# Kernel tuning notes

Measured on AMD Instinct MI355X. Metric: run time of the kernel, lower is better.

The kernel has to match this reference:

```python
import jax, jax.numpy as jnp
import numpy as np

B, L, D = 1, 4096, 1024
N_AR, N_DIFF, D_HEAD = 8, 8, 64
H = N_AR + N_DIFF
ROPE_BASE = 10000.0


def rotate_half(x):
    x1, x2 = jnp.split(x, 2, axis=-1)
    return jnp.concatenate([-x2, x1], axis=-1)


def rope_cos_sin(seq_len, d_head):
    inv_freq = 1.0 / (ROPE_BASE ** (jnp.arange(0, d_head, 2, dtype=jnp.float32) / d_head))
    t = jnp.arange(seq_len, dtype=jnp.float32)
    freqs = t[:, None] * inv_freq[None, :]          # [L, d_head//2]
    emb = jnp.concatenate([freqs, freqs], axis=-1)  # [L, d_head]
    return jnp.cos(emb), jnp.sin(emb)


def setup_inputs() -> dict:
    key = jax.random.key(0)
    ks = jax.random.split(key, 5)
    return {
        "hidden_states": jax.random.normal(ks[0], (B, L, D), dtype=jnp.float32),
        "Wq": jax.random.normal(ks[1], (D, H * D_HEAD), dtype=jnp.float32) * 0.02,
        "Wk": jax.random.normal(ks[2], (D, H * D_HEAD), dtype=jnp.float32) * 0.02,
        "Wv": jax.random.normal(ks[3], (D, H * D_HEAD), dtype=jnp.float32) * 0.02,
        "Wo": jax.random.normal(ks[4], (H * D_HEAD, D), dtype=jnp.float32) * 0.02,
    }


def _attend(q, k, v, mask):
    # q,k,v: [B, h, L, d]; mask: [L, L] additive
    scale = D_HEAD ** -0.5
    scores = jnp.einsum("bhqd,bhkd->bhqk", q, k) * scale + mask
    attn = jax.nn.softmax(scores.astype(jnp.float32), axis=-1).astype(q.dtype)
    return jnp.einsum("bhqk,bhkd->bhqd", attn, v)


def reference(hidden_states, Wq, Wk, Wv, Wo):
    b, l, _ = hidden_states.shape

    def heads(x, W):
        return (x @ W).reshape(b, l, H, D_HEAD).transpose(0, 2, 1, 3)  # [B,H,L,d]

    q = heads(hidden_states, Wq)
    k = heads(hidden_states, Wk)
    v = heads(hidden_states, Wv)

    cos, sin = rope_cos_sin(l, D_HEAD)  # [L, d]
    q = q * cos + rotate_half(q) * sin
    k = k * cos + rotate_half(k) * sin

    neg_inf = jnp.finfo(jnp.float32).min
    causal = jnp.where(jnp.tril(jnp.ones((l, l), dtype=bool)), 0.0, -jnp.inf).astype(jnp.float32)

    out_ar = _attend(q[:, :N_AR], k[:, :N_AR], v[:, :N_AR], causal)
    out_diff = _attend(q[:, N_AR:], k[:, N_AR:], v[:, N_AR:], jnp.zeros((l, l), jnp.float32))

    out = jnp.concatenate([out_ar, out_diff], axis=1)          # [B,H,L,d]
    out = out.transpose(0, 2, 1, 3).reshape(b, l, H * D_HEAD)  # [B,L,H*d]
    return out @ Wo
```

## Files before the change

kernel.cpp:

```cpp
#include <hip/hip_runtime.h>

#define LSEQ 4096
#define DMODEL 1024
#define HTOT 16
#define NAR 8
#define DHEAD 64
#define QKVS 3072

typedef unsigned short u16;
typedef unsigned int u32;
typedef __attribute__((ext_vector_type(8))) short bf16x8;
typedef __attribute__((ext_vector_type(4))) float f32x4;

typedef __attribute__((address_space(1))) void gvoid;
typedef __attribute__((address_space(3))) void lvoid;

__device__ __forceinline__ void cp16(const void* g, void* l) {
    __builtin_amdgcn_global_load_lds((gvoid*)(void*)g, (lvoid*)l, 16, 0, 0);
}

__device__ __forceinline__ float bfs(u16 v) { return __uint_as_float((u32)v << 16); }
__device__ __forceinline__ u16 f2bf(float f) {
    u32 x = __float_as_uint(f);
    return (u16)((x + 0x7fffu + ((x >> 16) & 1u)) >> 16);
}
__device__ __forceinline__ u32 pack2(float a, float b) {
    return (u32)f2bf(a) | ((u32)f2bf(b) << 16);
}

__global__ __launch_bounds__(256) void transp_cvt3(
    const float* __restrict__ Wq, const float* __restrict__ Wk,
    const float* __restrict__ Wv, u16* __restrict__ D)
{
    __shared__ u16 T[64][72];
    const float* S = (blockIdx.z == 0) ? Wq : ((blockIdx.z == 1) ? Wk : Wv);
    u16* Dz = D + (size_t)blockIdx.z * 1024 * 1024;
    const int tid = threadIdx.x;
    const int bx = blockIdx.x, by = blockIdx.y;
#pragma unroll
    for (int i = 0; i < 4; ++i) {
        int id = tid + i * 256;
        int fr = id >> 4, fc = id & 15;
        float4 v = *(const float4*)(S + (size_t)(by * 64 + fr) * 1024 + bx * 64 + fc * 4);
        T[fc * 4 + 0][fr] = f2bf(v.x);
        T[fc * 4 + 1][fr] = f2bf(v.y);
        T[fc * 4 + 2][fr] = f2bf(v.z);
        T[fc * 4 + 3][fr] = f2bf(v.w);
    }
    __syncthreads();
#pragma unroll
    for (int i = 0; i < 2; ++i) {
        int id = tid + i * 256;
        int c = id >> 3, g = id & 7;
        *(uint4*)(Dz + (size_t)(bx * 64 + c) * 1024 + by * 64 + g * 8) = *(const uint4*)&T[c][g * 8];
    }
}

__global__ __launch_bounds__(256) void transp_cvt(
    const float* __restrict__ S, u16* __restrict__ D)
{
    __shared__ u16 T[64][72];
    const int tid = threadIdx.x;
    const int bx = blockIdx.x, by = blockIdx.y;
#pragma unroll
    for (int i = 0; i < 4; ++i) {
        int id = tid + i * 256;
        int fr = id >> 4, fc = id & 15;
        float4 v = *(const float4*)(S + (size_t)(by * 64 + fr) * 1024 + bx * 64 + fc * 4);
        T[fc * 4 + 0][fr] = f2bf(v.x);
        T[fc * 4 + 1][fr] = f2bf(v.y);
        T[fc * 4 + 2][fr] = f2bf(v.z);
        T[fc * 4 + 3][fr] = f2bf(v.w);
    }
    __syncthreads();
#pragma unroll
    for (int i = 0; i < 2; ++i) {
        int id = tid + i * 256;
        int c = id >> 3, g = id & 7;
        *(uint4*)(D + (size_t)(bx * 64 + c) * 1024 + by * 64 + g * 8) = *(const uint4*)&T[c][g * 8];
    }
}

__global__ __launch_bounds__(256) void gemm_qkv(
    const float* __restrict__ A, const u16* __restrict__ Bt, u16* __restrict__ C)
{
    __shared__ u16 As[2][128][40];
    __shared__ u16 Bs[2][128][32];
    const int tid = threadIdx.x;
    const int lane = tid & 63, w = tid >> 6;
    const int col = lane & 15, quad = lane >> 4;
    const int bm = blockIdx.y << 7, bn = blockIdx.x << 7;
    const int wm = (w & 1) << 6, wn = (w >> 1) << 6;
    const int sr = lane >> 2, sc = (lane & 3) << 3;
    const int ar0 = tid >> 2, ag = (tid & 3) << 3;
    const f32x4 zero = {0.f, 0.f, 0.f, 0.f};
    f32x4 acc[4][4];
#pragma unroll
    for (int i = 0; i < 4; ++i)
#pragma unroll
        for (int j = 0; j < 4; ++j) acc[i][j] = zero;

    {
#pragma unroll
        for (int i = 0; i < 2; ++i)
            cp16(Bt + (size_t)(bn + w * 32 + i * 16 + sr) * 1024 + sc, &Bs[0][w * 32 + i * 16][0]);
        float4 a0[2], a1[2];
#pragma unroll
        for (int it = 0; it < 2; ++it) {
            const float* ap = A + (size_t)(bm + ar0 + it * 64) * 1024 + ag;
            a0[it] = *(const float4*)ap;
            a1[it] = *(const float4*)(ap + 4);
        }
#pragma unroll
        for (int it = 0; it < 2; ++it) {
            uint4 pk;
            pk.x = pack2(a0[it].x, a0[it].y); pk.y = pack2(a0[it].z, a0[it].w);
            pk.z = pack2(a1[it].x, a1[it].y); pk.w = pack2(a1[it].z, a1[it].w);
            *(uint4*)&As[0][ar0 + it * 64][ag] = pk;
        }
    }

    for (int kc = 0; kc < 32; ++kc) {
        const int cur = kc & 1, nxt = cur ^ 1;
        __syncthreads();
        const bool pre = (kc + 1 < 32);
        float4 a0[2], a1[2];
        if (pre) {
            const int k1 = (kc + 1) * 32;
#pragma unroll
            for (int i = 0; i < 2; ++i)
                cp16(Bt + (size_t)(bn + w * 32 + i * 16 + sr) * 1024 + k1 + sc,
                     &Bs[nxt][w * 32 + i * 16][0]);
#pragma unroll
            for (int it = 0; it < 2; ++it) {
                const float* ap = A + (size_t)(bm + ar0 + it * 64) * 1024 + k1 + ag;
                a0[it] = *(const float4*)ap;
                a1[it] = *(const float4*)(ap + 4);
            }
        }
        bf16x8 af[4], bfr[4];
#pragma unroll
        for (int i = 0; i < 4; ++i) af[i] = *(const bf16x8*)&As[cur][wm + i * 16 + col][quad * 8];
#pragma unroll
        for (int j = 0; j < 4; ++j) bfr[j] = *(const bf16x8*)&Bs[cur][wn + j * 16 + col][quad * 8];
#pragma unroll
        for (int i = 0; i < 4; ++i)
#pragma unroll
            for (int j = 0; j < 4; ++j)
                acc[i][j] = __builtin_amdgcn_mfma_f32_16x16x32_bf16(af[i], bfr[j], acc[i][j], 0, 0, 0);
        if (pre) {
#pragma unroll
            for (int it = 0; it < 2; ++it) {
                uint4 pk;
                pk.x = pack2(a0[it].x, a0[it].y); pk.y = pack2(a0[it].z, a0[it].w);
                pk.z = pack2(a1[it].x, a1[it].y); pk.w = pack2(a1[it].z, a1[it].w);
                *(uint4*)&As[nxt][ar0 + it * 64][ag] = pk;
            }
        }
    }
#pragma unroll
    for (int i = 0; i < 4; ++i)
#pragma unroll
        for (int j = 0; j < 4; ++j)
#pragma unroll
            for (int r = 0; r < 4; ++r)
                C[(size_t)(bm + wm + i * 16 + quad * 4 + r) * QKVS + bn + wn + j * 16 + col] =
                    f2bf(acc[i][j][r]);
}

__global__ __launch_bounds__(256) void gemm_out(
    const u16* __restrict__ A, const u16* __restrict__ Bt, float* __restrict__ C)
{
    __shared__ u16 As[2][128][32];
    __shared__ u16 Bs[2][128][32];
    const int tid = threadIdx.x;
    const int lane = tid & 63, w = tid >> 6;
    const int col = lane & 15, quad = lane >> 4;
    const int bm = blockIdx.y << 7, bn = blockIdx.x << 7;
    const int wm = (w & 1) << 6, wn = (w >> 1) << 6;
    const int sr = lane >> 2, sc = (lane & 3) << 3;
    const f32x4 zero = {0.f, 0.f, 0.f, 0.f};
    f32x4 acc[4][4];
#pragma unroll
    for (int i = 0; i < 4; ++i)
#pragma unroll
        for (int j = 0; j < 4; ++j) acc[i][j] = zero;

#pragma unroll
    for (int i = 0; i < 2; ++i) {
        const int r0 = w * 32 + i * 16;
        cp16(A  + (size_t)(bm + r0 + sr) * 1024 + sc, &As[0][r0][0]);
        cp16(Bt + (size_t)(bn + r0 + sr) * 1024 + sc, &Bs[0][r0][0]);
    }

    for (int kc = 0; kc < 32; ++kc) {
        const int cur = kc & 1, nxt = cur ^ 1;
        __syncthreads();
        if (kc + 1 < 32) {
            const int k1 = (kc + 1) * 32;
#pragma unroll
            for (int i = 0; i < 2; ++i) {
                const int r0 = w * 32 + i * 16;
                cp16(A  + (size_t)(bm + r0 + sr) * 1024 + k1 + sc, &As[nxt][r0][0]);
                cp16(Bt + (size_t)(bn + r0 + sr) * 1024 + k1 + sc, &Bs[nxt][r0][0]);
            }
        }
        bf16x8 af[4], bfr[4];
#pragma unroll
        for (int i = 0; i < 4; ++i) af[i] = *(const bf16x8*)&As[cur][wm + i * 16 + col][quad * 8];
#pragma unroll
        for (int j = 0; j < 4; ++j) bfr[j] = *(const bf16x8*)&Bs[cur][wn + j * 16 + col][quad * 8];
#pragma unroll
        for (int i = 0; i < 4; ++i)
#pragma unroll
            for (int j = 0; j < 4; ++j)
                acc[i][j] = __builtin_amdgcn_mfma_f32_16x16x32_bf16(af[i], bfr[j], acc[i][j], 0, 0, 0);
    }
#pragma unroll
    for (int i = 0; i < 4; ++i)
#pragma unroll
        for (int j = 0; j < 4; ++j)
#pragma unroll
            for (int r = 0; r < 4; ++r)
                C[(size_t)(bm + wm + i * 16 + quad * 4 + r) * 1024 + bn + wn + j * 16 + col] =
                    acc[i][j][r];
}

__global__ __launch_bounds__(256) void rope_kernel(u16* __restrict__ QKV)
{
    const int idx = blockIdx.x * 256 + threadIdx.x;
    const int i = idx & 31;
    const int h = (idx >> 5) & 15;
    const int t = idx >> 9;
    const float inv = __expf((float)i * -0.2878231366242557f);
    float s, c;
    __sincosf((float)t * inv, &s, &c);
    const size_t base = (size_t)t * QKVS + h * DHEAD + i;
    const float qs = 0.18033688011112042f;

    float q1 = bfs(QKV[base]), q2 = bfs(QKV[base + 32]);
    QKV[base]      = f2bf((q1 * c - q2 * s) * qs);
    QKV[base + 32] = f2bf((q2 * c + q1 * s) * qs);

    const size_t kb = base + 1024;
    float k1 = bfs(QKV[kb]), k2 = bfs(QKV[kb + 32]);
    QKV[kb]      = f2bf(k1 * c - k2 * s);
    QKV[kb + 32] = f2bf(k2 * c + k1 * s);
}

__global__ __launch_bounds__(256) void attn_mfma(
    const u16* __restrict__ QKV, u16* __restrict__ AO)
{
    __shared__ u16 Ks[2][64][64];
    __shared__ u16 Vt[2][80][72];
    __shared__ u16 Ps[4][32][72];
    const int bid = blockIdx.x;
    int h, qt;
    if (bid < 256) { h = 8 + (bid & 7); qt = bid >> 3; }
    else { int i = bid - 256; h = i & 7; qt = 31 - (i >> 3); }
    const bool causal = (h < NAR);
    const int tid = threadIdx.x;
    const int w = tid >> 6, lane = tid & 63;
    const int col = lane & 15, quad = lane >> 4;
    const int qbase = qt * 128 + w * 32;

    {
        int row = 64 + (tid >> 4);
        u32 val = (row == 64) ? 0x3F803F80u : 0u;
        u32* p0 = (u32*)&Vt[0][row][(tid & 15) * 4];
        u32* p1 = (u32*)&Vt[1][row][(tid & 15) * 4];
        p0[0] = val; p0[1] = val; p1[0] = val; p1[1] = val;
    }

    bf16x8 qf[2][2];
#pragma unroll
    for (int im = 0; im < 2; ++im)
#pragma unroll
        for (int ks = 0; ks < 2; ++ks)
            qf[im][ks] = *(const bf16x8*)(QKV + (size_t)(qbase + im * 16 + col) * QKVS +
                                          h * DHEAD + ks * 32 + quad * 8);

    const f32x4 zero = {0.f, 0.f, 0.f, 0.f};
    f32x4 O[2][5];
#pragma unroll
    for (int im = 0; im < 2; ++im)
#pragma unroll
        for (int nd = 0; nd < 5; ++nd) O[im][nd] = zero;

    const int nch = causal ? (qt * 2 + 2) : (LSEQ / 64);
    const int kv_kp = tid & 31, kv_dg = tid >> 5;
    u16* pb = &Ps[w][quad * 4][col];
    const int krow = lane >> 3;
    const int kcb = (lane & 7) ^ krow;
    const u16* kbase = QKV + (size_t)krow * QKVS + 1024 + h * DHEAD + kcb * 8;

    {
#pragma unroll
        for (int i = 0; i < 2; ++i)
            cp16(kbase + (size_t)((i * 4 + w) * 8) * QKVS, &Ks[0][(i * 4 + w) * 8][0]);
        const u16* vp = QKV + (size_t)(kv_kp * 2) * QKVS + 2048 + h * DHEAD + kv_dg * 8;
        bf16x8 v0 = *(const bf16x8*)vp;
        bf16x8 v1 = *(const bf16x8*)(vp + QKVS);
#pragma unroll
        for (int j = 0; j < 8; ++j)
            *(u32*)&Vt[0][kv_dg * 8 + j][kv_kp * 2] = (u32)(u16)v0[j] | ((u32)(u16)v1[j] << 16);
    }

    for (int ch = 0; ch < nch; ++ch) {
        const int cur = ch & 1, nxt = cur ^ 1;
        __syncthreads();
        const bool pre = (ch + 1 < nch);
        bf16x8 v0 = {}, v1 = {};
        if (pre) {
            const int c1 = (ch + 1) * 64;
#pragma unroll
            for (int i = 0; i < 2; ++i)
                cp16(kbase + (size_t)(c1 + (i * 4 + w) * 8) * QKVS, &Ks[nxt][(i * 4 + w) * 8][0]);
            const u16* vp = QKV + (size_t)(c1 + kv_kp * 2) * QKVS + 2048 + h * DHEAD + kv_dg * 8;
            v0 = *(const bf16x8*)vp;
            v1 = *(const bf16x8*)(vp + QKVS);
        }

        f32x4 s[2][4];
#pragma unroll
        for (int im = 0; im < 2; ++im)
#pragma unroll
            for (int jn = 0; jn < 4; ++jn) s[im][jn] = zero;
#pragma unroll
        for (int jn = 0; jn < 4; ++jn)
#pragma unroll
            for (int ks = 0; ks < 2; ++ks) {
                bf16x8 kf = *(const bf16x8*)&Ks[cur][jn * 16 + col][((ks * 4 + quad) ^ (col & 7)) * 8];
                s[0][jn] = __builtin_amdgcn_mfma_f32_16x16x32_bf16(qf[0][ks], kf, s[0][jn], 0, 0, 0);
                s[1][jn] = __builtin_amdgcn_mfma_f32_16x16x32_bf16(qf[1][ks], kf, s[1][jn], 0, 0, 0);
            }
        if (causal && ch * 64 + 63 > qbase) {
#pragma unroll
            for (int im = 0; im < 2; ++im)
#pragma unroll
                for (int jn = 0; jn < 4; ++jn) {
                    int kk = ch * 64 + jn * 16 + col;
#pragma unroll
                    for (int r = 0; r < 4; ++r) {
                        int qq = qbase + im * 16 + quad * 4 + r;
                        if (kk > qq) s[im][jn][r] = -1e30f;
                    }
                }
        }
#pragma unroll
        for (int im = 0; im < 2; ++im)
#pragma unroll
            for (int jn = 0; jn < 4; ++jn)
#pragma unroll
                for (int r = 0; r < 4; ++r)
                    pb[(im * 16 + r) * 72 + jn * 16] =
                        f2bf(__builtin_amdgcn_exp2f(s[im][jn][r]));
#pragma unroll
        for (int ks = 0; ks < 2; ++ks) {
            bf16x8 pa0 = *(const bf16x8*)&Ps[w][col][ks * 32 + quad * 8];
            bf16x8 pa1 = *(const bf16x8*)&Ps[w][16 + col][ks * 32 + quad * 8];
#pragma unroll
            for (int nd = 0; nd < 5; ++nd) {
                bf16x8 vf = *(const bf16x8*)&Vt[cur][nd * 16 + col][ks * 32 + quad * 8];
                O[0][nd] = __builtin_amdgcn_mfma_f32_16x16x32_bf16(pa0, vf, O[0][nd], 0, 0, 0);
                O[1][nd] = __builtin_amdgcn_mfma_f32_16x16x32_bf16(pa1, vf, O[1][nd], 0, 0, 0);
            }
        }
        if (pre) {
#pragma unroll
            for (int j = 0; j < 8; ++j)
                *(u32*)&Vt[nxt][kv_dg * 8 + j][kv_kp * 2] =
                    (u32)(u16)v0[j] | ((u32)(u16)v1[j] << 16);
        }
    }
#pragma unroll
    for (int im = 0; im < 2; ++im)
#pragma unroll
        for (int r = 0; r < 4; ++r) {
            float l = __shfl(O[im][4][r], 0, 16);
            float inv = 1.f / l;
            int row = im * 16 + quad * 4 + r;
#pragma unroll
            for (int nd = 0; nd < 4; ++nd)
                Ps[w][row][nd * 16 + col] = f2bf(O[im][nd][r] * inv);
        }
#pragma unroll
    for (int i = 0; i < 4; ++i) {
        int id = lane + i * 64;
        int row = id >> 3, g = id & 7;
        *(uint4*)(AO + (size_t)(qt * 128 + w * 32 + row) * 1024 + h * DHEAD + g * 8) =
            *(const uint4*)&Ps[w][row][g * 8];
    }
}

extern "C" void kernel_launch(void* const* d_in, const int* in_sizes, int n_in,
                              void* d_out, int out_size, void* d_ws, size_t ws_size,
                              hipStream_t stream)
{
    const float* X  = (const float*)d_in[0];
    const float* Wq = (const float*)d_in[1];
    const float* Wk = (const float*)d_in[2];
    const float* Wv = (const float*)d_in[3];
    const float* Wo = (const float*)d_in[4];
    float* out = (float*)d_out;

    u16* Wt  = (u16*)d_ws;
    u16* AOb = (u16*)d_ws;
    u16* QKV = (u16*)d_ws + (size_t)4 * 1024 * 1024;
    u16* Wot = QKV;

    transp_cvt3<<<dim3(16, 16, 3), 256, 0, stream>>>(Wq, Wk, Wv, Wt);
    gemm_qkv<<<dim3(24, 32), 256, 0, stream>>>(X, Wt, QKV);
    rope_kernel<<<(LSEQ * HTOT * 32) / 256, 256, 0, stream>>>(QKV);
    attn_mfma<<<512, 256, 0, stream>>>(QKV, AOb);
    transp_cvt<<<dim3(16, 16), 256, 0, stream>>>(Wo, Wot);
    gemm_out<<<dim3(8, 32), 256, 0, stream>>>(AOb, Wot, out);
}
```

Measured before the change: 292.9 us.

## Compute transposed scores to keep P in registers, halve query tile per block

The attention kernel now computes S^T = K·Q^T, so each lane holds the probabilities in the B-operand layout of the 16x16x16 MFMA. P·V then runs straight from registers, with no shared-memory staging of P and no LDS round trip for the output. Each block now covers 64 queries (16 per wave) instead of 128, doubling the grid to 1024 blocks. Causal tiles are ordered in alternating short/long pairs to balance load. The row sum is computed by an MFMA against a ones vector. In exchange, each K/V tile loaded into shared memory is reused by fewer queries, so global-to-LDS traffic per query roughly doubles.

```diff
diff --git a/kernel.cpp b/kernel.cpp
--- a/kernel.cpp
+++ b/kernel.cpp
@@ -10,6 +10,7 @@
 typedef unsigned short u16;
 typedef unsigned int u32;
 typedef __attribute__((ext_vector_type(8))) short bf16x8;
+typedef __attribute__((ext_vector_type(4))) short bf16x4;
 typedef __attribute__((ext_vector_type(4))) float f32x4;
 
 typedef __attribute__((address_space(1))) void gvoid;
@@ -252,44 +253,37 @@
     const u16* __restrict__ QKV, u16* __restrict__ AO)
 {
     __shared__ u16 Ks[2][64][64];
-    __shared__ u16 Vt[2][80][72];
-    __shared__ u16 Ps[4][32][72];
+    __shared__ u16 Vt[2][64][72];
     const int bid = blockIdx.x;
     int h, qt;
-    if (bid < 256) { h = 8 + (bid & 7); qt = bid >> 3; }
-    else { int i = bid - 256; h = i & 7; qt = 31 - (i >> 3); }
+    if (bid < 512) { h = 8 + (bid & 7); qt = bid >> 3; }
+    else {
+        int i = bid - 512; h = i & 7; int j = i >> 3;
+        qt = (j & 1) ? (63 - (j >> 1)) : (j >> 1);
+    }
     const bool causal = (h < NAR);
     const int tid = threadIdx.x;
     const int w = tid >> 6, lane = tid & 63;
     const int col = lane & 15, quad = lane >> 4;
-    const int qbase = qt * 128 + w * 32;
-
-    {
-        int row = 64 + (tid >> 4);
-        u32 val = (row == 64) ? 0x3F803F80u : 0u;
-        u32* p0 = (u32*)&Vt[0][row][(tid & 15) * 4];
-        u32* p1 = (u32*)&Vt[1][row][(tid & 15) * 4];
-        p0[0] = val; p0[1] = val; p1[0] = val; p1[1] = val;
-    }
-
-    bf16x8 qf[2][2];
-#pragma unroll
-    for (int im = 0; im < 2; ++im)
-#pragma unroll
-        for (int ks = 0; ks < 2; ++ks)
-            qf[im][ks] = *(const bf16x8*)(QKV + (size_t)(qbase + im * 16 + col) * QKVS +
-                                          h * DHEAD + ks * 32 + quad * 8);
+    const int qb = qt * 64;
+    const int qrow = qb + w * 16 + col;
+
+    bf16x8 qf[2];
+#pragma unroll
+    for (int ks = 0; ks < 2; ++ks)
+        qf[ks] = *(const bf16x8*)(QKV + (size_t)qrow * QKVS + h * DHEAD + ks * 32 + quad * 8);
+
+    bf16x4 ones;
+    ones[0] = (short)0x3F80; ones[1] = (short)0x3F80;
+    ones[2] = (short)0x3F80; ones[3] = (short)0x3F80;
 
     const f32x4 zero = {0.f, 0.f, 0.f, 0.f};
-    f32x4 O[2][5];
-#pragma unroll
-    for (int im = 0; im < 2; ++im)
-#pragma unroll
-        for (int nd = 0; nd < 5; ++nd) O[im][nd] = zero;
-
-    const int nch = causal ? (qt * 2 + 2) : (LSEQ / 64);
+    f32x4 O[5];
+#pragma unroll
+    for (int nd = 0; nd < 5; ++nd) O[nd] = zero;
+
+    const int nch = causal ? (qt + 1) : (LSEQ / 64);
     const int kv_kp = tid & 31, kv_dg = tid >> 5;
-    u16* pb = &Ps[w][quad * 4][col];
     const int krow = lane >> 3;
     const int kcb = (lane & 7) ^ krow;
     const u16* kbase = QKV + (size_t)krow * QKVS + 1024 + h * DHEAD + kcb * 8;
@@ -321,51 +315,44 @@
             v1 = *(const bf16x8*)(vp + QKVS);
         }
 
-        f32x4 s[2][4];
-#pragma unroll
-        for (int im = 0; im < 2; ++im)
-#pragma unroll
-            for (int jn = 0; jn < 4; ++jn) s[im][jn] = zero;
+        f32x4 st[4];
+#pragma unroll
+        for (int jn = 0; jn < 4; ++jn) st[jn] = zero;
 #pragma unroll
         for (int jn = 0; jn < 4; ++jn)
 #pragma unroll
             for (int ks = 0; ks < 2; ++ks) {
                 bf16x8 kf = *(const bf16x8*)&Ks[cur][jn * 16 + col][((ks * 4 + quad) ^ (col & 7)) * 8];
-                s[0][jn] = __builtin_amdgcn_mfma_f32_16x16x32_bf16(qf[0][ks], kf, s[0][jn], 0, 0, 0);
-                s[1][jn] = __builtin_amdgcn_mfma_f32_16x16x32_bf16(qf[1][ks], kf, s[1][jn], 0, 0, 0);
-            }
-        if (causal && ch * 64 + 63 > qbase) {
-#pragma unroll
-            for (int im = 0; im < 2; ++im)
-#pragma unroll
-                for (int jn = 0; jn < 4; ++jn) {
-                    int kk = ch * 64 + jn * 16 + col;
-#pragma unroll
-                    for (int r = 0; r < 4; ++r) {
-                        int qq = qbase + im * 16 + quad * 4 + r;
-                        if (kk > qq) s[im][jn][r] = -1e30f;
-                    }
-                }
-        }
-#pragma unroll
-        for (int im = 0; im < 2; ++im)
-#pragma unroll
-            for (int jn = 0; jn < 4; ++jn)
+                st[jn] = __builtin_amdgcn_mfma_f32_16x16x32_bf16(kf, qf[ks], st[jn], 0, 0, 0);
+            }
+        if (causal && ch * 64 + 63 > qb + w * 16) {
+#pragma unroll
+            for (int jn = 0; jn < 4; ++jn) {
+                int kk = ch * 64 + jn * 16 + quad * 4;
 #pragma unroll
                 for (int r = 0; r < 4; ++r)
-                    pb[(im * 16 + r) * 72 + jn * 16] =
-                        f2bf(__builtin_amdgcn_exp2f(s[im][jn][r]));
-#pragma unroll
-        for (int ks = 0; ks < 2; ++ks) {
-            bf16x8 pa0 = *(const bf16x8*)&Ps[w][col][ks * 32 + quad * 8];
-            bf16x8 pa1 = *(const bf16x8*)&Ps[w][16 + col][ks * 32 + quad * 8];
-#pragma unroll
-            for (int nd = 0; nd < 5; ++nd) {
-                bf16x8 vf = *(const bf16x8*)&Vt[cur][nd * 16 + col][ks * 32 + quad * 8];
-                O[0][nd] = __builtin_amdgcn_mfma_f32_16x16x32_bf16(pa0, vf, O[0][nd], 0, 0, 0);
-                O[1][nd] = __builtin_amdgcn_mfma_f32_16x16x32_bf16(pa1, vf, O[1][nd], 0, 0, 0);
-            }
-        }
+                    if (kk + r > qrow) st[jn][r] = -1e30f;
+            }
+        }
+        bf16x4 pf[4];
+#pragma unroll
+        for (int jn = 0; jn < 4; ++jn) {
+            pf[jn][0] = (short)f2bf(__builtin_amdgcn_exp2f(st[jn][0]));
+            pf[jn][1] = (short)f2bf(__builtin_amdgcn_exp2f(st[jn][1]));
+            pf[jn][2] = (short)f2bf(__builtin_amdgcn_exp2f(st[jn][2]));
+            pf[jn][3] = (short)f2bf(__builtin_amdgcn_exp2f(st[jn][3]));
+        }
+#pragma unroll
+        for (int nd = 0; nd < 4; ++nd)
+#pragma unroll
+            for (int jn = 0; jn < 4; ++jn) {
+                bf16x4 vtf = *(const bf16x4*)&Vt[cur][nd * 16 + col][jn * 16 + quad * 4];
+                O[nd] = __builtin_amdgcn_mfma_f32_16x16x16bf16_1k(vtf, pf[jn], O[nd], 0, 0, 0);
+            }
+#pragma unroll
+        for (int jn = 0; jn < 4; ++jn)
+            O[4] = __builtin_amdgcn_mfma_f32_16x16x16bf16_1k(ones, pf[jn], O[4], 0, 0, 0);
+
         if (pre) {
 #pragma unroll
             for (int j = 0; j < 8; ++j)
@@ -373,23 +360,15 @@
                     (u32)(u16)v0[j] | ((u32)(u16)v1[j] << 16);
         }
     }
-#pragma unroll
-    for (int im = 0; im < 2; ++im)
-#pragma unroll
-        for (int r = 0; r < 4; ++r) {
-            float l = __shfl(O[im][4][r], 0, 16);
-            float inv = 1.f / l;
-            int row = im * 16 + quad * 4 + r;
-#pragma unroll
-            for (int nd = 0; nd < 4; ++nd)
-                Ps[w][row][nd * 16 + col] = f2bf(O[im][nd][r] * inv);
-        }
-#pragma unroll
-    for (int i = 0; i < 4; ++i) {
-        int id = lane + i * 64;
-        int row = id >> 3, g = id & 7;
-        *(uint4*)(AO + (size_t)(qt * 128 + w * 32 + row) * 1024 + h * DHEAD + g * 8) =
-            *(const uint4*)&Ps[w][row][g * 8];
+    const float inv = 1.f / O[4][0];
+#pragma unroll
+    for (int nd = 0; nd < 4; ++nd) {
+        ushort4 ov;
+        ov.x = f2bf(O[nd][0] * inv);
+        ov.y = f2bf(O[nd][1] * inv);
+        ov.z = f2bf(O[nd][2] * inv);
+        ov.w = f2bf(O[nd][3] * inv);
+        *(ushort4*)(AO + (size_t)qrow * 1024 + h * DHEAD + nd * 16 + quad * 4) = ov;
     }
 }
 
@@ -412,7 +391,7 @@
     transp_cvt3<<<dim3(16, 16, 3), 256, 0, stream>>>(Wq, Wk, Wv, Wt);
     gemm_qkv<<<dim3(24, 32), 256, 0, stream>>>(X, Wt, QKV);
     rope_kernel<<<(LSEQ * HTOT * 32) / 256, 256, 0, stream>>>(QKV);
-    attn_mfma<<<512, 256, 0, stream>>>(QKV, AOb);
+    attn_mfma<<<1024, 256, 0, stream>>>(QKV, AOb);
     transp_cvt<<<dim3(16, 16), 256, 0, stream>>>(Wo, Wot);
     gemm_out<<<dim3(8, 32), 256, 0, stream>>>(AOb, Wot, out);
 }
```

Result: faster. 275.1 us (-6.1%).
